# Kernel tuning notes

Hardware: AMD Instinct MI355X
Metric: run time of the kernel (lower is better)

Reference implementation:

```python
import jax, jax.numpy as jnp
import numpy as np

NUM_LAYERS = 4
EPS = 1e-8


def setup_inputs() -> dict:
    key = jax.random.key(0)
    ks = jax.random.split(key, 7)
    N, D, H = 8192, 1024, 4096
    return {
        "x": jax.random.normal(ks[0], (N, D), jnp.float32),
        "fc1_W": jax.random.normal(ks[1], (H, D), jnp.float32) * 0.02,
        "fc1_b": jax.random.normal(ks[2], (H,), jnp.float32) * 0.02,
        "fc2_W": jax.random.normal(ks[3], (D, H), jnp.float32) * 0.02,
        "fc2_b": jax.random.normal(ks[4], (D,), jnp.float32) * 0.02,
        "comp_W": jax.random.normal(ks[5], (NUM_LAYERS + 1, D, D), jnp.float32) * 0.03,
        "comp_b": jax.random.normal(ks[6], (NUM_LAYERS + 1, D), jnp.float32) * 0.03,
    }


def _block(x, fc1_W, fc1_b, fc2_W, fc2_b):
    # fc2(dropout(fc1(x))) in eval mode; relu is defined but never applied
    h = x @ fc1_W.T + fc1_b
    return h @ fc2_W.T + fc2_b


def _compute_loss(z, W, b):
    # out = Linear(z); per-row cosine_similarity(out_i.unsqueeze(1), out_i.unsqueeze(0))
    # reduces broadcast dim 1 -> vector c[j] = out[j]*sum(out) / max(|out[j]|*sqrt(y)*||out||, eps)
    # which torch broadcasts into constant rows of a [y,y] matrix; the
    # abs-diff accumulation over batch rows is then rank-1.
    out = z @ W.T + b                                # [N, y]
    y = out.shape[-1]
    S = out.sum(-1, keepdims=True)                   # [N, 1]
    n2 = jnp.sqrt((out * out).sum(-1, keepdims=True))  # [N, 1] row norms
    n1 = jnp.abs(out) * jnp.sqrt(jnp.asarray(y, out.dtype))  # [N, y]
    c = out * S / jnp.maximum(n1 * n2, EPS)          # [N, y]
    D = jnp.abs(c[1:] - c[:-1]).sum(0)               # [y]
    return jnp.broadcast_to(D, (y, y))               # [y, y]


def reference(x, fc1_W, fc1_b, fc2_W, fc2_b, comp_W, comp_b):
    inv = _block(x, fc1_W, fc1_b, fc2_W, fc2_b)
    loss = _compute_loss(inv, comp_W[0], comp_b[0])
    nxt = x - inv
    inv_total = inv
    for i in range(1, NUM_LAYERS + 1):
        inv_new = _block(nxt, fc1_W, fc1_b, fc2_W, fc2_b)
        inv_total = inv_total + inv_new
        loss = loss + _compute_loss(inv_new, comp_W[i], comp_b[i])
        nxt = nxt - inv_new
    return inv_total, nxt, loss
```

## Files before the change

kernel.cpp:

```cpp
#include <hip/hip_runtime.h>
#include <hip/hip_bf16.h>


#define NR 8192
#define DD 1024
#define HH 4096
#define NL 5
#define MSZ (DD * DD)

using bf16 = __hip_bfloat16;
typedef __attribute__((ext_vector_type(8))) short bf16x8;
typedef __attribute__((ext_vector_type(4))) float f32x4;


__device__ __forceinline__ void cvt4(const float* __restrict__ in, bf16* __restrict__ out, int i) {
  float4 v = ((const float4*)in)[i];
  union { bf16 b[4]; uint2 u; } u;
  u.b[0] = __float2bfloat16(v.x); u.b[1] = __float2bfloat16(v.y);
  u.b[2] = __float2bfloat16(v.z); u.b[3] = __float2bfloat16(v.w);
  ((uint2*)out)[i] = u.u;
}

#define NX4 (NR * DD / 4)
#define NF4 (DD * HH / 4)
#define NC4 (NL * MSZ / 4)
#define NS4 ((NL * DD + 2 * NL * NR) / 4)
#define NE4 (DD)

__global__ void prep_kernel(const float* __restrict__ x, const float* __restrict__ fc2_W,
                            const float* __restrict__ comp_W,
                            bf16* __restrict__ x_bf, bf16* __restrict__ fc2_bf,
                            bf16* __restrict__ compW_bf,
                            float* __restrict__ stats, float* __restrict__ ebuf) {
  int i = blockIdx.x * 256 + threadIdx.x;
  const int stride = gridDim.x * 256;
  const int total = NX4 + NF4 + NC4 + NS4 + NE4;
  const float4 z4 = {0.f, 0.f, 0.f, 0.f};
  for (; i < total; i += stride) {
    if (i < NX4) cvt4(x, x_bf, i);
    else if (i < NX4 + NF4) cvt4(fc2_W, fc2_bf, i - NX4);
    else if (i < NX4 + NF4 + NC4) cvt4(comp_W, compW_bf, i - NX4 - NF4);
    else if (i < NX4 + NF4 + NC4 + NS4) ((float4*)stats)[i - NX4 - NF4 - NC4] = z4;
    else ((float4*)ebuf)[i - NX4 - NF4 - NC4 - NS4] = z4;
  }
}

__global__ void transpose_cvt_kernel(const float* __restrict__ in, bf16* __restrict__ out) {
  __shared__ bf16 tile[64][74];
  int c0 = blockIdx.x * 64;
  int r0 = blockIdx.y * 64;
  int col = threadIdx.x & 63;
  int row4 = threadIdx.x >> 6;
  #pragma unroll
  for (int j = 0; j < 16; ++j) {
    int r = row4 * 16 + j;
    tile[r][col] = __float2bfloat16(in[(size_t)(r0 + r) * DD + c0 + col]);
  }
  __syncthreads();
  #pragma unroll
  for (int j = 0; j < 16; ++j) {
    int r = row4 * 16 + j;
    out[(size_t)(c0 + r) * HH + r0 + col] = tile[col][r];
  }
}

__global__ void cvec_kernel(const float* __restrict__ fc1_b, const float* __restrict__ fc2_W,
                            const float* __restrict__ fc2_b, float* __restrict__ c) {
  int j = blockIdx.x;
  float s = 0.f;
  for (int k = threadIdx.x; k < HH; k += 256) s += fc1_b[k] * fc2_W[(size_t)j * HH + k];
  for (int o = 32; o; o >>= 1) s += __shfl_down(s, o);
  __shared__ float red[4];
  if ((threadIdx.x & 63) == 0) red[threadIdx.x >> 6] = s;
  __syncthreads();
  if (threadIdx.x == 0) c[j] = red[0] + red[1] + red[2] + red[3] + fc2_b[j];
}

__global__ void mbuild_kernel(const float* __restrict__ Cp,
                              bf16* __restrict__ M, bf16* __restrict__ T, bf16* __restrict__ Tt) {
  __shared__ float tile[64][65];
  int n0 = blockIdx.x * 64, m0 = blockIdx.y * 64;
  int tn = threadIdx.x & 63, tm4 = threadIdx.x >> 6;
  #pragma unroll
  for (int j = 0; j < 16; ++j) {
    int m = tm4 * 16 + j;
    size_t idx = (size_t)(m0 + m) * DD + n0 + tn;
    float v = Cp[idx] + Cp[MSZ + idx] + Cp[2 * MSZ + idx] + Cp[3 * MSZ + idx];
    tile[m][tn] = v;
    float d = ((m0 + m) == (n0 + tn)) ? 1.f : 0.f;
    M[idx] = __float2bfloat16(v);
    T[idx] = __float2bfloat16(d - v);
  }
  __syncthreads();
  #pragma unroll
  for (int j = 0; j < 16; ++j) {
    int r = tm4 * 16 + j;
    float v = tile[tn][r];
    size_t idx = (size_t)(n0 + r) * DD + m0 + tn;
    float d = ((n0 + r) == (m0 + tn)) ? 1.f : 0.f;
    Tt[idx] = __float2bfloat16(d - v);
  }
}

__global__ void gemv4_kernel(const float* __restrict__ c, const bf16* __restrict__ Pw,
                             float* __restrict__ ebuf) {
  const int z = blockIdx.y;
  const int j = blockIdx.x * 256 + threadIdx.x;
  const bf16* P = Pw + (size_t)z * MSZ + j;
  const int k0 = blockIdx.z * 256;
  float s = 0.f;
  #pragma unroll 8
  for (int k = k0; k < k0 + 256; ++k) s += c[k] * __bfloat162float(P[(size_t)k * DD]);
  atomicAdd(&ebuf[z * DD + j], s);
}

__global__ void biasall_kernel(const float* __restrict__ cvec, const float* __restrict__ ebuf,
                               const float* __restrict__ comp_W, const float* __restrict__ comp_b,
                               float* __restrict__ biasall) {
  int z = blockIdx.y, j = blockIdx.x;
  if (z == 0) {
    if (threadIdx.x == 0)
      biasall[j] = cvec[j] + ebuf[j] + ebuf[DD + j] + ebuf[2 * DD + j] + ebuf[3 * DD + j];
    return;
  }
  int i = z - 1;
  const float* e = (i == 0) ? cvec : ebuf + (size_t)(i - 1) * DD;
  const float* wr = comp_W + (size_t)i * MSZ + (size_t)j * DD;
  float s = 0.f;
  for (int k = threadIdx.x; k < DD; k += 256) s += e[k] * wr[k];
  for (int o = 32; o; o >>= 1) s += __shfl_down(s, o);
  __shared__ float red[4];
  if ((threadIdx.x & 63) == 0) red[threadIdx.x >> 6] = s;
  __syncthreads();
  if (threadIdx.x == 0)
    biasall[(size_t)z * DD + j] = red[0] + red[1] + red[2] + red[3] + comp_b[(size_t)i * DD + j];
}


__device__ __forceinline__ void async16(const bf16* g, bf16* l) {
  __builtin_amdgcn_global_load_lds(
      (const __attribute__((address_space(1))) void*)g,
      (__attribute__((address_space(3))) void*)l, 16, 0, 0);
}

__device__ __forceinline__ void gemm_core_async(
    const bf16* __restrict__ A, const bf16* __restrict__ B,
    int kBeg, int kEnd, int lda, int ldb, int bm, int bn,
    bf16* As, bf16* Bs, f32x4 acc[4][4])
{
  const int tid  = threadIdx.x;
  const int lane = tid & 63;
  const int wave = tid >> 6;
  const int wm = (wave & 1) * 64;
  const int wn = (wave >> 1) * 64;
  const int lr = lane >> 3;
  const int lcol = ((lane & 7) ^ lr) * 8;
  const bf16* gA = A + (size_t)(bm + wave * 32 + lr) * lda + lcol;
  const bf16* gB = B + (size_t)(bn + wave * 32 + lr) * ldb + lcol;
  bf16* lA = As + wave * 32 * 64;
  bf16* lB = Bs + wave * 32 * 64;

  for (int k0 = kBeg; k0 < kEnd; k0 += 64) {
    #pragma unroll
    for (int it = 0; it < 4; ++it) {
      async16(gA + (size_t)(it * 8) * lda + k0, lA + it * 8 * 64);
      async16(gB + (size_t)(it * 8) * ldb + k0, lB + it * 8 * 64);
    }
    __syncthreads();
    #pragma unroll
    for (int ks = 0; ks < 2; ++ks) {
      bf16x8 av[4], bv[4];
      #pragma unroll
      for (int i = 0; i < 4; ++i) {
        const int rr = i * 16 + (lane & 15);
        const int cc = ((ks * 4 + (lane >> 4)) ^ (lane & 7)) * 8;
        av[i] = *(const bf16x8*)(As + (wm + rr) * 64 + cc);
        bv[i] = *(const bf16x8*)(Bs + (wn + rr) * 64 + cc);
      }
      #pragma unroll
      for (int i = 0; i < 4; ++i)
        #pragma unroll
        for (int j = 0; j < 4; ++j)
          acc[i][j] = __builtin_amdgcn_mfma_f32_16x16x32_bf16(av[i], bv[j], acc[i][j], 0, 0, 0);
    }
    __syncthreads();
  }
}

__device__ __forceinline__ void gemm_core64(
    const bf16* __restrict__ A, const bf16* __restrict__ B,
    int kBeg, int kEnd, int lda, int ldb, int bm, int bn,
    bf16* As, bf16* Bs, f32x4 acc[2][2])
{
  const int tid  = threadIdx.x;
  const int lane = tid & 63;
  const int wave = tid >> 6;
  const int wm = (wave & 1) * 32;
  const int wn = (wave >> 1) * 32;
  const int lr = lane >> 3;
  const int lcol = ((lane & 7) ^ lr) * 8;
  const bf16* gA = A + (size_t)(bm + wave * 16 + lr) * lda + lcol;
  const bf16* gB = B + (size_t)(bn + wave * 16 + lr) * ldb + lcol;
  bf16* lA = As + wave * 16 * 64;
  bf16* lB = Bs + wave * 16 * 64;

  for (int k0 = kBeg; k0 < kEnd; k0 += 64) {
    #pragma unroll
    for (int it = 0; it < 2; ++it) {
      async16(gA + (size_t)(it * 8) * lda + k0, lA + it * 8 * 64);
      async16(gB + (size_t)(it * 8) * ldb + k0, lB + it * 8 * 64);
    }
    __syncthreads();
    #pragma unroll
    for (int ks = 0; ks < 2; ++ks) {
      bf16x8 av[2], bv[2];
      #pragma unroll
      for (int i = 0; i < 2; ++i) {
        const int rr = i * 16 + (lane & 15);
        const int cc = ((ks * 4 + (lane >> 4)) ^ (lane & 7)) * 8;
        av[i] = *(const bf16x8*)(As + (wm + rr) * 64 + cc);
        bv[i] = *(const bf16x8*)(Bs + (wn + rr) * 64 + cc);
      }
      #pragma unroll
      for (int i = 0; i < 2; ++i)
        #pragma unroll
        for (int j = 0; j < 2; ++j)
          acc[i][j] = __builtin_amdgcn_mfma_f32_16x16x32_bf16(av[i], bv[j], acc[i][j], 0, 0, 0);
    }
    __syncthreads();
  }
}

#define GEMM_PROLOGUE \
  alignas(16) __shared__ bf16 As[128 * 64]; \
  alignas(16) __shared__ bf16 Bs[128 * 64]; \
  f32x4 acc[4][4] = {}; \
  const int lane = threadIdx.x & 63; \
  const int wm = ((threadIdx.x >> 6) & 1) * 64; \
  const int wn = ((threadIdx.x >> 6) >> 1) * 64;

#define GEMM_PROLOGUE64 \
  alignas(16) __shared__ bf16 As[64 * 64]; \
  alignas(16) __shared__ bf16 Bs[64 * 64]; \
  f32x4 acc[2][2] = {}; \
  const int lane = threadIdx.x & 63; \
  const int wm = ((threadIdx.x >> 6) & 1) * 32; \
  const int wn = ((threadIdx.x >> 6) >> 1) * 32;

__global__ __launch_bounds__(256, 4)
void gemm_splitk64(const bf16* __restrict__ A, const bf16* __restrict__ B, float* __restrict__ Cp) {
  GEMM_PROLOGUE64
  const int bm = blockIdx.y * 64, bn = blockIdx.x * 64;
  const int kb = blockIdx.z * (HH / 4);
  gemm_core64(A, B, kb, kb + HH / 4, HH, HH, bm, bn, As, Bs, acc);
  float* C = Cp + (size_t)blockIdx.z * MSZ;
  #pragma unroll
  for (int i = 0; i < 2; ++i)
    #pragma unroll
    for (int j = 0; j < 2; ++j) {
      const int col = bn + wn + j * 16 + (lane & 15);
      #pragma unroll
      for (int r = 0; r < 4; ++r) {
        const int row = bm + wm + i * 16 + (lane >> 4) * 4 + r;
        C[(size_t)row * DD + col] = acc[i][j][r];
      }
    }
}

__global__ __launch_bounds__(256, 4)
void gemm_dual64(const bf16* __restrict__ A, const bf16* __restrict__ B,
                 bf16* __restrict__ Ct, bf16* __restrict__ Cn) {
  GEMM_PROLOGUE64
  const int bm = blockIdx.y * 64, bn = blockIdx.x * 64;
  gemm_core64(A, B, 0, DD, DD, DD, bm, bn, As, Bs, acc);
  #pragma unroll
  for (int i = 0; i < 2; ++i)
    #pragma unroll
    for (int j = 0; j < 2; ++j) {
      const int col = bn + wn + j * 16 + (lane & 15);
      const int row0 = bm + wm + i * 16 + (lane >> 4) * 4;
      union { bf16 b[4]; uint2 u; } pk;
      #pragma unroll
      for (int r = 0; r < 4; ++r) {
        bf16 v = __float2bfloat16(acc[i][j][r]);
        pk.b[r] = v;
        Cn[(size_t)(row0 + r) * DD + col] = v;
      }
      *(uint2*)(&Ct[(size_t)col * DD + row0]) = pk.u;
    }
}

__global__ __launch_bounds__(256, 4)
void gemm_b64(const bf16* __restrict__ A0, long astr, const bf16* __restrict__ B0, long bstr,
              bf16* __restrict__ C0, long cstr) {
  GEMM_PROLOGUE64
  const int z = blockIdx.z;
  const bf16* A = A0 + (size_t)z * astr;
  const bf16* B = B0 + (size_t)z * bstr;
  bf16* C = C0 + (size_t)z * cstr;
  const int bm = blockIdx.y * 64, bn = blockIdx.x * 64;
  gemm_core64(A, B, 0, DD, DD, DD, bm, bn, As, Bs, acc);
  #pragma unroll
  for (int i = 0; i < 2; ++i)
    #pragma unroll
    for (int j = 0; j < 2; ++j) {
      const int col = bn + wn + j * 16 + (lane & 15);
      #pragma unroll
      for (int r = 0; r < 4; ++r) {
        const int row = bm + wm + i * 16 + (lane >> 4) * 4 + r;
        C[(size_t)row * DD + col] = __float2bfloat16(acc[i][j][r]);
      }
    }
}

__global__ __launch_bounds__(256, 4)
void gemm_t5_64(const bf16* __restrict__ A, const bf16* __restrict__ B,
                const bf16* __restrict__ Pw, bf16* __restrict__ Dl, bf16* __restrict__ Bbig0) {
  GEMM_PROLOGUE64
  const int bm = blockIdx.y * 64, bn = blockIdx.x * 64;
  gemm_core64(A, B, 0, DD, DD, DD, bm, bn, As, Bs, acc);
  #pragma unroll
  for (int i = 0; i < 2; ++i)
    #pragma unroll
    for (int j = 0; j < 2; ++j) {
      const int col = bn + wn + j * 16 + (lane & 15);
      const int row0 = bm + wm + i * 16 + (lane >> 4) * 4;
      union { bf16 b[4]; uint2 u; } pk;
      #pragma unroll
      for (int r = 0; r < 4; ++r) {
        const size_t idx = (size_t)(row0 + r) * DD + col;
        const float t1 = __bfloat162float(Pw[idx]);
        const float t2 = __bfloat162float(Pw[MSZ + idx]);
        const float t3 = __bfloat162float(Pw[2 * MSZ + idx]);
        const float t4 = __bfloat162float(Pw[3 * MSZ + idx]);
        const float t5 = acc[i][j][r];
        Dl[idx]           = __float2bfloat16(t1 - t2);
        Dl[MSZ + idx]     = __float2bfloat16(t2 - t3);
        Dl[2 * MSZ + idx] = __float2bfloat16(t3 - t4);
        Dl[3 * MSZ + idx] = __float2bfloat16(t4 - t5);
        pk.b[r] = __float2bfloat16((((row0 + r) == col) ? 1.f : 0.f) - t5);
      }
      *(uint2*)(&Bbig0[(size_t)col * DD + row0]) = pk.u;
    }
}

__global__ __launch_bounds__(256, 2)
void gemm_main(const bf16* __restrict__ A, const bf16* __restrict__ Bb,
               const float* __restrict__ biasall, const bf16* __restrict__ xb,
               float* __restrict__ invtot, float* __restrict__ nxtf,
               unsigned long long* __restrict__ sgn,
               float* __restrict__ Srow, float* __restrict__ Qrow) {
  GEMM_PROLOGUE
  const int bm = blockIdx.y * 128, bn = blockIdx.x * 128;
  gemm_core_async(A, Bb + (size_t)(bn >> 10) * MSZ, 0, DD, DD, DD, bm, bn & (DD - 1), As, Bs, acc);

  if (bn < DD) {
    #pragma unroll
    for (int i = 0; i < 4; ++i)
      #pragma unroll
      for (int j = 0; j < 4; ++j) {
        const int col = bn + wn + j * 16 + (lane & 15);
        const float bj = biasall[col];
        #pragma unroll
        for (int r = 0; r < 4; ++r) {
          const int row = bm + wm + i * 16 + (lane >> 4) * 4 + r;
          const float v = acc[i][j][r] + bj;
          const size_t idx = (size_t)row * DD + col;
          invtot[idx] = v;
          nxtf[idx] = __bfloat162float(xb[idx]) - v;
        }
      }
  } else {
    const int z = (bn >> 10) - 1;
    const int rb = bm >> 7;
    const int cb = (bn & (DD - 1)) >> 7;
    const int wave = threadIdx.x >> 6;
    unsigned long long keep = 0ULL;
    float sv[4][4] = {}, qv[4][4] = {};
    #pragma unroll
    for (int i = 0; i < 4; ++i)
      #pragma unroll
      for (int j = 0; j < 4; ++j) {
        const int colg = bn + wn + j * 16 + (lane & 15);
        const float bj = biasall[colg];
        #pragma unroll
        for (int r = 0; r < 4; ++r) {
          const float v = acc[i][j][r] + bj;
          const unsigned long long bal = __ballot(v < 0.f);
          if (lane == i * 16 + j * 4 + r) keep = bal;
          sv[i][r] += v;
          qv[i][r] += v * v;
        }
      }
    const size_t wbase = ((((size_t)z * 64 + rb) * 8 + cb) * 4 + wave) * 64;
    sgn[wbase + lane] = keep;
    #pragma unroll
    for (int i = 0; i < 4; ++i)
      #pragma unroll
      for (int r = 0; r < 4; ++r) {
        float s = sv[i][r], q = qv[i][r];
        #pragma unroll
        for (int off = 1; off < 16; off <<= 1) { s += __shfl_xor(s, off); q += __shfl_xor(q, off); }
        if ((lane & 15) == 0) {
          const int row = bm + wm + i * 16 + (lane >> 4) * 4 + r;
          atomicAdd(&Srow[(size_t)z * NR + row], s);
          atomicAdd(&Qrow[(size_t)z * NR + row], q);
        }
      }
  }
}


__global__ void losssign_kernel(const unsigned long long* __restrict__ sgn,
                                const float* __restrict__ Srow, const float* __restrict__ Qrow,
                                float* __restrict__ Dtot) {
  const int z = blockIdx.y;
  const int cg = blockIdx.x;
  const int n0 = blockIdx.z * 1024;
  __shared__ float rsh[1025];
  const float* S = Srow + (size_t)z * NR;
  const float* Q = Qrow + (size_t)z * NR;
  for (int t = threadIdx.x; t < 1025; t += 256) {
    int n = n0 + t; if (n > NR - 1) n = NR - 1;
    rsh[t] = S[n] * rsqrtf(Q[n]) * 0.03125f;
  }
  __syncthreads();
  const int c = threadIdx.x & 63;
  const int q = threadIdx.x >> 6;
  const int col = cg * 64 + c;
  const int cb = col >> 7;
  const int wsel = (col >> 6) & 1;
  const int jf = (col >> 4) & 3;
  const int c15 = col & 15;
  const size_t zbase = (size_t)z * 64 * 8 * 4 * 64;
  const int ns = n0 + q * 256;
  int ne = ns + 256; if (ne > NR - 1) ne = NR - 1;

  auto cval = [&](int n) -> float {
    const int rbk = n >> 7, nl = n & 127;
    const int wave = (nl >> 6) | (wsel << 1);
    const int i = (nl >> 4) & 3, rg = (nl >> 2) & 3, r = nl & 3;
    const size_t widx = zbase + ((((size_t)rbk * 8 + cb) * 4 + wave) * 64)
                      + i * 16 + jf * 4 + r;
    const unsigned long long wv = sgn[widx];
    const float rv = rsh[n - n0];
    return ((wv >> (rg * 16 + c15)) & 1ULL) ? -rv : rv;
  };

  float d = 0.f;
  float cprev = cval(ns);
  for (int n = ns + 1; n <= ne; ++n) {
    const float cn = cval(n);
    d += fabsf(cn - cprev);
    cprev = cn;
  }
  atomicAdd(&Dtot[z * DD + col], d);
}

__global__ void writeloss_kernel(const float* __restrict__ Dtot, float* __restrict__ out) {
  int idx = blockIdx.x * 256 + threadIdx.x;
  int j = idx & (DD - 1);
  out[idx] = Dtot[j] + Dtot[DD + j] + Dtot[2 * DD + j] + Dtot[3 * DD + j] + Dtot[4 * DD + j];
}


extern "C" void kernel_launch(void* const* d_in, const int* in_sizes, int n_in,
                              void* d_out, int out_size, void* d_ws, size_t ws_size,
                              hipStream_t stream) {
  const float* x      = (const float*)d_in[0];
  const float* fc1_W  = (const float*)d_in[1];
  const float* fc1_b  = (const float*)d_in[2];
  const float* fc2_W  = (const float*)d_in[3];
  const float* fc2_b  = (const float*)d_in[4];
  const float* comp_W = (const float*)d_in[5];
  const float* comp_b = (const float*)d_in[6];

  float* invtot  = (float*)d_out;
  float* nxtf    = invtot + (size_t)NR * DD;
  float* lossout = invtot + (size_t)2 * NR * DD;

  char* w = (char*)d_ws;
  auto alloc = [&](size_t bytes) { char* p = w; w += (bytes + 255) & ~(size_t)255; return p; };
  bf16* x_bf     = (bf16*)alloc((size_t)NR * DD * 2);
  bf16* fc1T_bf  = (bf16*)alloc((size_t)DD * HH * 2);
  bf16* fc2_bf   = (bf16*)alloc((size_t)DD * HH * 2);
  bf16* compW_bf = (bf16*)alloc((size_t)NL * MSZ * 2);
  bf16* Dbank    = (bf16*)alloc((size_t)5 * MSZ * 2);
  bf16* M_bf = Dbank;
  bf16* Dl   = Dbank + MSZ;
  bf16* Tt_buf   = (bf16*)alloc((size_t)2 * MSZ * 2);
  bf16* Pw       = (bf16*)alloc((size_t)4 * MSZ * 2);
  bf16* Bbig     = (bf16*)alloc((size_t)6 * MSZ * 2);
  unsigned long long* sgn = (unsigned long long*)alloc((size_t)NL * 64 * 8 * 4 * 64 * 8);
  float* Cp      = (float*)alloc((size_t)4 * MSZ * 4);
  float* cvec    = (float*)alloc(DD * 4);
  float* ebuf    = (float*)alloc((size_t)4 * DD * 4);
  float* biasall = (float*)alloc((size_t)6 * DD * 4);
  float* stats   = (float*)alloc((size_t)(NL * DD + 2 * NL * NR) * 4);
  float* Dtot = stats;
  float* Srow = stats + NL * DD;
  float* Qrow = Srow + (size_t)NL * NR;
  (void)ws_size; (void)in_sizes; (void)n_in; (void)out_size;

  prep_kernel<<<2048, 256, 0, stream>>>(x, fc2_W, comp_W, x_bf, fc2_bf, compW_bf, stats, ebuf);
  transpose_cvt_kernel<<<dim3(DD / 64, HH / 64), 256, 0, stream>>>(fc1_W, fc1T_bf);
  cvec_kernel<<<DD, 256, 0, stream>>>(fc1_b, fc2_W, fc2_b, cvec);

  gemm_splitk64<<<dim3(16, 16, 4), 256, 0, stream>>>(fc1T_bf, fc2_bf, Cp);
  mbuild_kernel<<<dim3(16, 16), 256, 0, stream>>>(Cp, M_bf, Pw, Tt_buf);
  gemm_dual64<<<dim3(16, 16), 256, 0, stream>>>(Pw, Tt_buf, Tt_buf + MSZ, Pw + MSZ);
  gemm_b64<<<dim3(16, 16, 2), 256, 0, stream>>>(Pw + MSZ, 0, Tt_buf, MSZ, Pw + 2 * MSZ, MSZ);
  gemm_t5_64<<<dim3(16, 16), 256, 0, stream>>>(Pw + 3 * MSZ, Tt_buf, Pw, Dl, Bbig);
  gemv4_kernel<<<dim3(4, 4, 4), 256, 0, stream>>>(cvec, Pw, ebuf);
  biasall_kernel<<<dim3(DD, 6), 256, 0, stream>>>(cvec, ebuf, comp_W, comp_b, biasall);
  gemm_b64<<<dim3(16, 16, NL), 256, 0, stream>>>(compW_bf, MSZ, Dbank, MSZ, Bbig + MSZ, MSZ);

  gemm_main<<<dim3(6 * DD / 128, NR / 128), 256, 0, stream>>>(
      x_bf, Bbig, biasall, x_bf, invtot, nxtf, sgn, Srow, Qrow);

  losssign_kernel<<<dim3(16, NL, 8), 256, 0, stream>>>(sgn, Srow, Qrow, Dtot);
  writeloss_kernel<<<MSZ / 256, 256, 0, stream>>>(Dtot, lossout);
}
```

Measured before the change: 483.1 us.

## Merge weight-precompute chain into one cooperative persistent kernel with grid syncs

Replaces the sequence of small weight-precompute kernels (split-K GEMM, M build, dual GEMM, batched GEMMs, t5 GEMM, gemv, bias) with a single cooperative kernel of 512 blocks separated by grid.sync, and merges the transpose and cvec kernels into one launch. The goal is to remove launch gaps and tail idle time between many short, under-occupied kernels and to overlap gemv/bias work with GEMM stages. Split-K for the first GEMM drops from 4 to 2 slices, which gives each block more serial work. The risk is that grid barriers and fixed per-block work assignment leave CUs idle where the separate launches could have packed more blocks.

```diff
diff --git a/kernel.cpp b/kernel.cpp
--- a/kernel.cpp
+++ b/kernel.cpp
@@ -1,5 +1,8 @@
 #include <hip/hip_runtime.h>
 #include <hip/hip_bf16.h>
+#include <hip/hip_cooperative_groups.h>
+
+namespace cg = cooperative_groups;
 
 
 #define NR 8192
@@ -45,95 +48,36 @@
   }
 }
 
-__global__ void transpose_cvt_kernel(const float* __restrict__ in, bf16* __restrict__ out) {
-  __shared__ bf16 tile[64][74];
-  int c0 = blockIdx.x * 64;
-  int r0 = blockIdx.y * 64;
-  int col = threadIdx.x & 63;
-  int row4 = threadIdx.x >> 6;
-  #pragma unroll
-  for (int j = 0; j < 16; ++j) {
-    int r = row4 * 16 + j;
-    tile[r][col] = __float2bfloat16(in[(size_t)(r0 + r) * DD + c0 + col]);
-  }
-  __syncthreads();
-  #pragma unroll
-  for (int j = 0; j < 16; ++j) {
-    int r = row4 * 16 + j;
-    out[(size_t)(c0 + r) * HH + r0 + col] = tile[col][r];
-  }
-}
-
-__global__ void cvec_kernel(const float* __restrict__ fc1_b, const float* __restrict__ fc2_W,
-                            const float* __restrict__ fc2_b, float* __restrict__ c) {
-  int j = blockIdx.x;
-  float s = 0.f;
-  for (int k = threadIdx.x; k < HH; k += 256) s += fc1_b[k] * fc2_W[(size_t)j * HH + k];
-  for (int o = 32; o; o >>= 1) s += __shfl_down(s, o);
-  __shared__ float red[4];
-  if ((threadIdx.x & 63) == 0) red[threadIdx.x >> 6] = s;
-  __syncthreads();
-  if (threadIdx.x == 0) c[j] = red[0] + red[1] + red[2] + red[3] + fc2_b[j];
-}
-
-__global__ void mbuild_kernel(const float* __restrict__ Cp,
-                              bf16* __restrict__ M, bf16* __restrict__ T, bf16* __restrict__ Tt) {
-  __shared__ float tile[64][65];
-  int n0 = blockIdx.x * 64, m0 = blockIdx.y * 64;
-  int tn = threadIdx.x & 63, tm4 = threadIdx.x >> 6;
-  #pragma unroll
-  for (int j = 0; j < 16; ++j) {
-    int m = tm4 * 16 + j;
-    size_t idx = (size_t)(m0 + m) * DD + n0 + tn;
-    float v = Cp[idx] + Cp[MSZ + idx] + Cp[2 * MSZ + idx] + Cp[3 * MSZ + idx];
-    tile[m][tn] = v;
-    float d = ((m0 + m) == (n0 + tn)) ? 1.f : 0.f;
-    M[idx] = __float2bfloat16(v);
-    T[idx] = __float2bfloat16(d - v);
-  }
-  __syncthreads();
-  #pragma unroll
-  for (int j = 0; j < 16; ++j) {
-    int r = tm4 * 16 + j;
-    float v = tile[tn][r];
-    size_t idx = (size_t)(n0 + r) * DD + m0 + tn;
-    float d = ((n0 + r) == (m0 + tn)) ? 1.f : 0.f;
-    Tt[idx] = __float2bfloat16(d - v);
-  }
-}
-
-__global__ void gemv4_kernel(const float* __restrict__ c, const bf16* __restrict__ Pw,
-                             float* __restrict__ ebuf) {
-  const int z = blockIdx.y;
-  const int j = blockIdx.x * 256 + threadIdx.x;
-  const bf16* P = Pw + (size_t)z * MSZ + j;
-  const int k0 = blockIdx.z * 256;
-  float s = 0.f;
-  #pragma unroll 8
-  for (int k = k0; k < k0 + 256; ++k) s += c[k] * __bfloat162float(P[(size_t)k * DD]);
-  atomicAdd(&ebuf[z * DD + j], s);
-}
-
-__global__ void biasall_kernel(const float* __restrict__ cvec, const float* __restrict__ ebuf,
-                               const float* __restrict__ comp_W, const float* __restrict__ comp_b,
-                               float* __restrict__ biasall) {
-  int z = blockIdx.y, j = blockIdx.x;
-  if (z == 0) {
-    if (threadIdx.x == 0)
-      biasall[j] = cvec[j] + ebuf[j] + ebuf[DD + j] + ebuf[2 * DD + j] + ebuf[3 * DD + j];
-    return;
-  }
-  int i = z - 1;
-  const float* e = (i == 0) ? cvec : ebuf + (size_t)(i - 1) * DD;
-  const float* wr = comp_W + (size_t)i * MSZ + (size_t)j * DD;
-  float s = 0.f;
-  for (int k = threadIdx.x; k < DD; k += 256) s += e[k] * wr[k];
-  for (int o = 32; o; o >>= 1) s += __shfl_down(s, o);
-  __shared__ float red[4];
-  if ((threadIdx.x & 63) == 0) red[threadIdx.x >> 6] = s;
-  __syncthreads();
-  if (threadIdx.x == 0)
-    biasall[(size_t)z * DD + j] = red[0] + red[1] + red[2] + red[3] + comp_b[(size_t)i * DD + j];
+__global__ void smallprep_kernel(const float* __restrict__ fc1_W, bf16* __restrict__ fc1T,
+                                 const float* __restrict__ fc1_b, const float* __restrict__ fc2_W,
+                                 const float* __restrict__ fc2_b, float* __restrict__ cvec) {
+  if (blockIdx.x < 1024) {
+    __shared__ bf16 tile[64][74];
+    const int c0 = (blockIdx.x & 15) * 64;
+    const int r0 = (blockIdx.x >> 4) * 64;
+    const int col = threadIdx.x & 63;
+    const int row4 = threadIdx.x >> 6;
+    #pragma unroll
+    for (int j = 0; j < 16; ++j) {
+      int r = row4 * 16 + j;
+      tile[r][col] = __float2bfloat16(fc1_W[(size_t)(r0 + r) * DD + c0 + col]);
+    }
+    __syncthreads();
+    #pragma unroll
+    for (int j = 0; j < 16; ++j) {
+      int r = row4 * 16 + j;
+      fc1T[(size_t)(c0 + r) * HH + r0 + col] = tile[col][r];
+    }
+  } else {
+    const int j = blockIdx.x - 1024;
+    float s = 0.f;
+    for (int k = threadIdx.x; k < HH; k += 256) s += fc1_b[k] * fc2_W[(size_t)j * HH + k];
+    for (int o = 32; o; o >>= 1) s += __shfl_down(s, o);
+    __shared__ float red[4];
+    if ((threadIdx.x & 63) == 0) red[threadIdx.x >> 6] = s;
+    __syncthreads();
+    if (threadIdx.x == 0) cvec[j] = red[0] + red[1] + red[2] + red[3] + fc2_b[j];
+  }
 }
 
 
@@ -142,6 +86,239 @@
       (const __attribute__((address_space(1))) void*)g,
       (__attribute__((address_space(3))) void*)l, 16, 0, 0);
 }
+
+__device__ __forceinline__ void gemm_core64(
+    const bf16* __restrict__ A, const bf16* __restrict__ B,
+    int kBeg, int kEnd, int lda, int ldb, int bm, int bn,
+    bf16* As, bf16* Bs, f32x4 acc[2][2])
+{
+  const int tid  = threadIdx.x;
+  const int lane = tid & 63;
+  const int wave = tid >> 6;
+  const int wm = (wave & 1) * 32;
+  const int wn = (wave >> 1) * 32;
+  const int lr = lane >> 3;
+  const int lcol = ((lane & 7) ^ lr) * 8;
+  const bf16* gA = A + (size_t)(bm + wave * 16 + lr) * lda + lcol;
+  const bf16* gB = B + (size_t)(bn + wave * 16 + lr) * ldb + lcol;
+  bf16* lA = As + wave * 16 * 64;
+  bf16* lB = Bs + wave * 16 * 64;
+
+  for (int k0 = kBeg; k0 < kEnd; k0 += 64) {
+    #pragma unroll
+    for (int it = 0; it < 2; ++it) {
+      async16(gA + (size_t)(it * 8) * lda + k0, lA + it * 8 * 64);
+      async16(gB + (size_t)(it * 8) * ldb + k0, lB + it * 8 * 64);
+    }
+    __syncthreads();
+    #pragma unroll
+    for (int ks = 0; ks < 2; ++ks) {
+      bf16x8 av[2], bv[2];
+      #pragma unroll
+      for (int i = 0; i < 2; ++i) {
+        const int rr = i * 16 + (lane & 15);
+        const int cc = ((ks * 4 + (lane >> 4)) ^ (lane & 7)) * 8;
+        av[i] = *(const bf16x8*)(As + (wm + rr) * 64 + cc);
+        bv[i] = *(const bf16x8*)(Bs + (wn + rr) * 64 + cc);
+      }
+      #pragma unroll
+      for (int i = 0; i < 2; ++i)
+        #pragma unroll
+        for (int j = 0; j < 2; ++j)
+          acc[i][j] = __builtin_amdgcn_mfma_f32_16x16x32_bf16(av[i], bv[j], acc[i][j], 0, 0, 0);
+    }
+    __syncthreads();
+  }
+}
+
+
+__global__ __launch_bounds__(256, 2)
+void mega_kernel(const bf16* __restrict__ fc1T, const bf16* __restrict__ fc2b,
+                 const float* __restrict__ cvec, const bf16* __restrict__ compWb,
+                 const float* __restrict__ comp_W, const float* __restrict__ comp_b,
+                 float* __restrict__ Cp, bf16* __restrict__ Dbank, bf16* __restrict__ Pw,
+                 bf16* __restrict__ Ttb, bf16* __restrict__ Bbig,
+                 float* __restrict__ ebuf, float* __restrict__ biasall) {
+  cg::grid_group grid = cg::this_grid();
+  __shared__ char smem[16640];
+  bf16* As = (bf16*)smem;
+  bf16* Bs = (bf16*)(smem + 8192);
+  const int b = blockIdx.x;
+  const int lane = threadIdx.x & 63;
+  const int wm = ((threadIdx.x >> 6) & 1) * 32;
+  const int wn = ((threadIdx.x >> 6) >> 1) * 32;
+
+  {
+    const int t = b >> 1, kh = b & 1;
+    const int m0 = (t >> 4) * 64, n0 = (t & 15) * 64;
+    f32x4 acc[2][2] = {};
+    gemm_core64(fc1T, fc2b, kh * (HH / 2), (kh + 1) * (HH / 2), HH, HH, m0, n0, As, Bs, acc);
+    float* C = Cp + (size_t)kh * MSZ;
+    #pragma unroll
+    for (int i = 0; i < 2; ++i)
+      #pragma unroll
+      for (int j = 0; j < 2; ++j) {
+        const int col = n0 + wn + j * 16 + (lane & 15);
+        #pragma unroll
+        for (int r = 0; r < 4; ++r) {
+          const int row = m0 + wm + i * 16 + (lane >> 4) * 4 + r;
+          C[(size_t)row * DD + col] = acc[i][j][r];
+        }
+      }
+  }
+  grid.sync();
+  if (b < 256) {
+    float (*tile)[65] = (float(*)[65])smem;
+    const int m0 = (b >> 4) * 64, n0 = (b & 15) * 64;
+    const int tn = threadIdx.x & 63, tm4 = threadIdx.x >> 6;
+    #pragma unroll
+    for (int j = 0; j < 16; ++j) {
+      const int m = tm4 * 16 + j;
+      const size_t idx = (size_t)(m0 + m) * DD + n0 + tn;
+      const float v = Cp[idx] + Cp[MSZ + idx];
+      tile[m][tn] = v;
+      const float d = ((m0 + m) == (n0 + tn)) ? 1.f : 0.f;
+      Dbank[idx] = __float2bfloat16(v);
+      Pw[idx]    = __float2bfloat16(d - v);
+    }
+    __syncthreads();
+    #pragma unroll
+    for (int j = 0; j < 16; ++j) {
+      const int r = tm4 * 16 + j;
+      const float v = tile[tn][r];
+      const size_t idx = (size_t)(n0 + r) * DD + m0 + tn;
+      const float d = ((n0 + r) == (m0 + tn)) ? 1.f : 0.f;
+      Ttb[idx] = __float2bfloat16(d - v);
+    }
+  }
+  grid.sync();
+  if (b < 256) {
+    const int m0 = (b >> 4) * 64, n0 = (b & 15) * 64;
+    f32x4 acc[2][2] = {};
+    gemm_core64(Pw, Ttb, 0, DD, DD, DD, m0, n0, As, Bs, acc);
+    #pragma unroll
+    for (int i = 0; i < 2; ++i)
+      #pragma unroll
+      for (int j = 0; j < 2; ++j) {
+        const int col = n0 + wn + j * 16 + (lane & 15);
+        const int row0 = m0 + wm + i * 16 + (lane >> 4) * 4;
+        union { bf16 h[4]; uint2 u; } pk;
+        #pragma unroll
+        for (int r = 0; r < 4; ++r) {
+          bf16 v = __float2bfloat16(acc[i][j][r]);
+          pk.h[r] = v;
+          Pw[MSZ + (size_t)(row0 + r) * DD + col] = v;
+        }
+        *(uint2*)(&Ttb[MSZ + (size_t)col * DD + row0]) = pk.u;
+      }
+  } else if (b < 272) {
+    const int idx = b - 256, jg = idx & 3, kg = idx >> 2;
+    const int j = jg * 256 + threadIdx.x, k0 = kg * 256;
+    float s = 0.f;
+    #pragma unroll 8
+    for (int k = k0; k < k0 + 256; ++k) s += cvec[k] * __bfloat162float(Pw[(size_t)k * DD + j]);
+    atomicAdd(&ebuf[j], s);
+  }
+  grid.sync();
+  {
+    const int z = b >> 8, t = b & 255;
+    const int m0 = (t >> 4) * 64, n0 = (t & 15) * 64;
+    f32x4 acc[2][2] = {};
+    gemm_core64(Pw + MSZ, Ttb + (size_t)z * MSZ, 0, DD, DD, DD, m0, n0, As, Bs, acc);
+    bf16* C = Pw + (size_t)(2 + z) * MSZ;
+    #pragma unroll
+    for (int i = 0; i < 2; ++i)
+      #pragma unroll
+      for (int j = 0; j < 2; ++j) {
+        const int col = n0 + wn + j * 16 + (lane & 15);
+        #pragma unroll
+        for (int r = 0; r < 4; ++r) {
+          const int row = m0 + wm + i * 16 + (lane >> 4) * 4 + r;
+          C[(size_t)row * DD + col] = __float2bfloat16(acc[i][j][r]);
+        }
+      }
+  }
+  grid.sync();
+  if (b < 256) {
+    const int m0 = (b >> 4) * 64, n0 = (b & 15) * 64;
+    f32x4 acc[2][2] = {};
+    gemm_core64(Pw + 3 * MSZ, Ttb, 0, DD, DD, DD, m0, n0, As, Bs, acc);
+    bf16* Dl = Dbank + MSZ;
+    #pragma unroll
+    for (int i = 0; i < 2; ++i)
+      #pragma unroll
+      for (int j = 0; j < 2; ++j) {
+        const int col = n0 + wn + j * 16 + (lane & 15);
+        const int row0 = m0 + wm + i * 16 + (lane >> 4) * 4;
+        union { bf16 h[4]; uint2 u; } pk;
+        #pragma unroll
+        for (int r = 0; r < 4; ++r) {
+          const size_t idx = (size_t)(row0 + r) * DD + col;
+          const float t1 = __bfloat162float(Pw[idx]);
+          const float t2 = __bfloat162float(Pw[MSZ + idx]);
+          const float t3 = __bfloat162float(Pw[2 * MSZ + idx]);
+          const float t4 = __bfloat162float(Pw[3 * MSZ + idx]);
+          const float t5 = acc[i][j][r];
+          Dl[idx]           = __float2bfloat16(t1 - t2);
+          Dl[MSZ + idx]     = __float2bfloat16(t2 - t3);
+          Dl[2 * MSZ + idx] = __float2bfloat16(t3 - t4);
+          Dl[3 * MSZ + idx] = __float2bfloat16(t4 - t5);
+          pk.h[r] = __float2bfloat16((((row0 + r) == col) ? 1.f : 0.f) - t5);
+        }
+        *(uint2*)(&Bbig[(size_t)col * DD + row0]) = pk.u;
+      }
+  } else if (b < 304) {
+    const int z = 1 + (b - 256) / 16, idx = (b - 256) % 16, jg = idx & 3, kg = idx >> 2;
+    const int j = jg * 256 + threadIdx.x, k0 = kg * 256;
+    const bf16* P = Pw + (size_t)z * MSZ;
+    float s = 0.f;
+    #pragma unroll 8
+    for (int k = k0; k < k0 + 256; ++k) s += cvec[k] * __bfloat162float(P[(size_t)k * DD + j]);
+    atomicAdd(&ebuf[(size_t)z * DD + j], s);
+  }
+  grid.sync();
+  for (int jb = b; jb < 1280; jb += 512) {
+    const int z = jb >> 8, t = jb & 255;
+    const int m0 = (t >> 4) * 64, n0 = (t & 15) * 64;
+    f32x4 acc[2][2] = {};
+    gemm_core64(compWb + (size_t)z * MSZ, Dbank + (size_t)z * MSZ, 0, DD, DD, DD,
+                m0, n0, As, Bs, acc);
+    bf16* C = Bbig + (size_t)(1 + z) * MSZ;
+    #pragma unroll
+    for (int i = 0; i < 2; ++i)
+      #pragma unroll
+      for (int j = 0; j < 2; ++j) {
+        const int col = n0 + wn + j * 16 + (lane & 15);
+        #pragma unroll
+        for (int r = 0; r < 4; ++r) {
+          const int row = m0 + wm + i * 16 + (lane >> 4) * 4 + r;
+          C[(size_t)row * DD + col] = __float2bfloat16(acc[i][j][r]);
+        }
+      }
+  }
+  float* red = (float*)smem;
+  for (int q = 0; q < 12; ++q) {
+    const int o = b * 12 + q;
+    const int z = o >> 10, j = o & 1023;
+    __syncthreads();
+    if (z == 0) {
+      if (threadIdx.x == 0)
+        biasall[j] = cvec[j] + ebuf[j] + ebuf[DD + j] + ebuf[2 * DD + j] + ebuf[3 * DD + j];
+    } else {
+      const int i = z - 1;
+      const float* e = (i == 0) ? cvec : ebuf + (size_t)(i - 1) * DD;
+      const float* wr2 = comp_W + (size_t)i * MSZ + (size_t)j * DD;
+      float s = 0.f;
+      for (int k = threadIdx.x; k < DD; k += 256) s += e[k] * wr2[k];
+      for (int o2 = 32; o2; o2 >>= 1) s += __shfl_down(s, o2);
+      if ((threadIdx.x & 63) == 0) red[threadIdx.x >> 6] = s;
+      __syncthreads();
+      if (threadIdx.x == 0)
+        biasall[(size_t)z * DD + j] = red[0] + red[1] + red[2] + red[3] + comp_b[(size_t)i * DD + j];
+    }
+  }
+}
+
 
 __device__ __forceinline__ void gemm_core_async(
     const bf16* __restrict__ A, const bf16* __restrict__ B,
@@ -187,50 +364,6 @@
   }
 }
 
-__device__ __forceinline__ void gemm_core64(
-    const bf16* __restrict__ A, const bf16* __restrict__ B,
-    int kBeg, int kEnd, int lda, int ldb, int bm, int bn,
-    bf16* As, bf16* Bs, f32x4 acc[2][2])
-{
-  const int tid  = threadIdx.x;
-  const int lane = tid & 63;
-  const int wave = tid >> 6;
-  const int wm = (wave & 1) * 32;
-  const int wn = (wave >> 1) * 32;
-  const int lr = lane >> 3;
-  const int lcol = ((lane & 7) ^ lr) * 8;
-  const bf16* gA = A + (size_t)(bm + wave * 16 + lr) * lda + lcol;
-  const bf16* gB = B + (size_t)(bn + wave * 16 + lr) * ldb + lcol;
-  bf16* lA = As + wave * 16 * 64;
-  bf16* lB = Bs + wave * 16 * 64;
-
-  for (int k0 = kBeg; k0 < kEnd; k0 += 64) {
-    #pragma unroll
-    for (int it = 0; it < 2; ++it) {
-      async16(gA + (size_t)(it * 8) * lda + k0, lA + it * 8 * 64);
-      async16(gB + (size_t)(it * 8) * ldb + k0, lB + it * 8 * 64);
-    }
-    __syncthreads();
-    #pragma unroll
-    for (int ks = 0; ks < 2; ++ks) {
-      bf16x8 av[2], bv[2];
-      #pragma unroll
-      for (int i = 0; i < 2; ++i) {
-        const int rr = i * 16 + (lane & 15);
-        const int cc = ((ks * 4 + (lane >> 4)) ^ (lane & 7)) * 8;
-        av[i] = *(const bf16x8*)(As + (wm + rr) * 64 + cc);
-        bv[i] = *(const bf16x8*)(Bs + (wn + rr) * 64 + cc);
-      }
-      #pragma unroll
-      for (int i = 0; i < 2; ++i)
-        #pragma unroll
-        for (int j = 0; j < 2; ++j)
-          acc[i][j] = __builtin_amdgcn_mfma_f32_16x16x32_bf16(av[i], bv[j], acc[i][j], 0, 0, 0);
-    }
-    __syncthreads();
-  }
-}
-
 #define GEMM_PROLOGUE \
   alignas(16) __shared__ bf16 As[128 * 64]; \
   alignas(16) __shared__ bf16 Bs[128 * 64]; \
@@ -238,111 +371,6 @@
   const int lane = threadIdx.x & 63; \
   const int wm = ((threadIdx.x >> 6) & 1) * 64; \
   const int wn = ((threadIdx.x >> 6) >> 1) * 64;
-
-#define GEMM_PROLOGUE64 \
-  alignas(16) __shared__ bf16 As[64 * 64]; \
-  alignas(16) __shared__ bf16 Bs[64 * 64]; \
-  f32x4 acc[2][2] = {}; \
-  const int lane = threadIdx.x & 63; \
-  const int wm = ((threadIdx.x >> 6) & 1) * 32; \
-  const int wn = ((threadIdx.x >> 6) >> 1) * 32;
-
-__global__ __launch_bounds__(256, 4)
-void gemm_splitk64(const bf16* __restrict__ A, const bf16* __restrict__ B, float* __restrict__ Cp) {
-  GEMM_PROLOGUE64
-  const int bm = blockIdx.y * 64, bn = blockIdx.x * 64;
-  const int kb = blockIdx.z * (HH / 4);
-  gemm_core64(A, B, kb, kb + HH / 4, HH, HH, bm, bn, As, Bs, acc);
-  float* C = Cp + (size_t)blockIdx.z * MSZ;
-  #pragma unroll
-  for (int i = 0; i < 2; ++i)
-    #pragma unroll
-    for (int j = 0; j < 2; ++j) {
-      const int col = bn + wn + j * 16 + (lane & 15);
-      #pragma unroll
-      for (int r = 0; r < 4; ++r) {
-        const int row = bm + wm + i * 16 + (lane >> 4) * 4 + r;
-        C[(size_t)row * DD + col] = acc[i][j][r];
-      }
-    }
-}
-
-__global__ __launch_bounds__(256, 4)
-void gemm_dual64(const bf16* __restrict__ A, const bf16* __restrict__ B,
-                 bf16* __restrict__ Ct, bf16* __restrict__ Cn) {
-  GEMM_PROLOGUE64
-  const int bm = blockIdx.y * 64, bn = blockIdx.x * 64;
-  gemm_core64(A, B, 0, DD, DD, DD, bm, bn, As, Bs, acc);
-  #pragma unroll
-  for (int i = 0; i < 2; ++i)
-    #pragma unroll
-    for (int j = 0; j < 2; ++j) {
-      const int col = bn + wn + j * 16 + (lane & 15);
-      const int row0 = bm + wm + i * 16 + (lane >> 4) * 4;
-      union { bf16 b[4]; uint2 u; } pk;
-      #pragma unroll
-      for (int r = 0; r < 4; ++r) {
-        bf16 v = __float2bfloat16(acc[i][j][r]);
-        pk.b[r] = v;
-        Cn[(size_t)(row0 + r) * DD + col] = v;
-      }
-      *(uint2*)(&Ct[(size_t)col * DD + row0]) = pk.u;
-    }
-}
-
-__global__ __launch_bounds__(256, 4)
-void gemm_b64(const bf16* __restrict__ A0, long astr, const bf16* __restrict__ B0, long bstr,
-              bf16* __restrict__ C0, long cstr) {
-  GEMM_PROLOGUE64
-  const int z = blockIdx.z;
-  const bf16* A = A0 + (size_t)z * astr;
-  const bf16* B = B0 + (size_t)z * bstr;
-  bf16* C = C0 + (size_t)z * cstr;
-  const int bm = blockIdx.y * 64, bn = blockIdx.x * 64;
-  gemm_core64(A, B, 0, DD, DD, DD, bm, bn, As, Bs, acc);
-  #pragma unroll
-  for (int i = 0; i < 2; ++i)
-    #pragma unroll
-    for (int j = 0; j < 2; ++j) {
-      const int col = bn + wn + j * 16 + (lane & 15);
-      #pragma unroll
-      for (int r = 0; r < 4; ++r) {
-        const int row = bm + wm + i * 16 + (lane >> 4) * 4 + r;
-        C[(size_t)row * DD + col] = __float2bfloat16(acc[i][j][r]);
-      }
-    }
-}
-
-__global__ __launch_bounds__(256, 4)
-void gemm_t5_64(const bf16* __restrict__ A, const bf16* __restrict__ B,
-                const bf16* __restrict__ Pw, bf16* __restrict__ Dl, bf16* __restrict__ Bbig0) {
-  GEMM_PROLOGUE64
-  const int bm = blockIdx.y * 64, bn = blockIdx.x * 64;
-  gemm_core64(A, B, 0, DD, DD, DD, bm, bn, As, Bs, acc);
-  #pragma unroll
-  for (int i = 0; i < 2; ++i)
-    #pragma unroll
-    for (int j = 0; j < 2; ++j) {
-      const int col = bn + wn + j * 16 + (lane & 15);
-      const int row0 = bm + wm + i * 16 + (lane >> 4) * 4;
-      union { bf16 b[4]; uint2 u; } pk;
-      #pragma unroll
-      for (int r = 0; r < 4; ++r) {
-        const size_t idx = (size_t)(row0 + r) * DD + col;
-        const float t1 = __bfloat162float(Pw[idx]);
-        const float t2 = __bfloat162float(Pw[MSZ + idx]);
-        const float t3 = __bfloat162float(Pw[2 * MSZ + idx]);
-        const float t4 = __bfloat162float(Pw[3 * MSZ + idx]);
-        const float t5 = acc[i][j][r];
-        Dl[idx]           = __float2bfloat16(t1 - t2);
-        Dl[MSZ + idx]     = __float2bfloat16(t2 - t3);
-        Dl[2 * MSZ + idx] = __float2bfloat16(t3 - t4);
-        Dl[3 * MSZ + idx] = __float2bfloat16(t4 - t5);
-        pk.b[r] = __float2bfloat16((((row0 + r) == col) ? 1.f : 0.f) - t5);
-      }
-      *(uint2*)(&Bbig0[(size_t)col * DD + row0]) = pk.u;
-    }
-}
 
 __global__ __launch_bounds__(256, 2)
 void gemm_main(const bf16* __restrict__ A, const bf16* __restrict__ Bb,
@@ -486,13 +514,11 @@
   bf16* fc2_bf   = (bf16*)alloc((size_t)DD * HH * 2);
   bf16* compW_bf = (bf16*)alloc((size_t)NL * MSZ * 2);
   bf16* Dbank    = (bf16*)alloc((size_t)5 * MSZ * 2);
-  bf16* M_bf = Dbank;
-  bf16* Dl   = Dbank + MSZ;
   bf16* Tt_buf   = (bf16*)alloc((size_t)2 * MSZ * 2);
   bf16* Pw       = (bf16*)alloc((size_t)4 * MSZ * 2);
   bf16* Bbig     = (bf16*)alloc((size_t)6 * MSZ * 2);
   unsigned long long* sgn = (unsigned long long*)alloc((size_t)NL * 64 * 8 * 4 * 64 * 8);
-  float* Cp      = (float*)alloc((size_t)4 * MSZ * 4);
+  float* Cp      = (float*)alloc((size_t)2 * MSZ * 4);
   float* cvec    = (float*)alloc(DD * 4);
   float* ebuf    = (float*)alloc((size_t)4 * DD * 4);
   float* biasall = (float*)alloc((size_t)6 * DD * 4);
@@ -503,21 +529,16 @@
   (void)ws_size; (void)in_sizes; (void)n_in; (void)out_size;
 
   prep_kernel<<<2048, 256, 0, stream>>>(x, fc2_W, comp_W, x_bf, fc2_bf, compW_bf, stats, ebuf);
-  transpose_cvt_kernel<<<dim3(DD / 64, HH / 64), 256, 0, stream>>>(fc1_W, fc1T_bf);
-  cvec_kernel<<<DD, 256, 0, stream>>>(fc1_b, fc2_W, fc2_b, cvec);
-
-  gemm_splitk64<<<dim3(16, 16, 4), 256, 0, stream>>>(fc1T_bf, fc2_bf, Cp);
-  mbuild_kernel<<<dim3(16, 16), 256, 0, stream>>>(Cp, M_bf, Pw, Tt_buf);
-  gemm_dual64<<<dim3(16, 16), 256, 0, stream>>>(Pw, Tt_buf, Tt_buf + MSZ, Pw + MSZ);
-  gemm_b64<<<dim3(16, 16, 2), 256, 0, stream>>>(Pw + MSZ, 0, Tt_buf, MSZ, Pw + 2 * MSZ, MSZ);
-  gemm_t5_64<<<dim3(16, 16), 256, 0, stream>>>(Pw + 3 * MSZ, Tt_buf, Pw, Dl, Bbig);
-  gemv4_kernel<<<dim3(4, 4, 4), 256, 0, stream>>>(cvec, Pw, ebuf);
-  biasall_kernel<<<dim3(DD, 6), 256, 0, stream>>>(cvec, ebuf, comp_W, comp_b, biasall);
-  gemm_b64<<<dim3(16, 16, NL), 256, 0, stream>>>(compW_bf, MSZ, Dbank, MSZ, Bbig + MSZ, MSZ);
-
+  smallprep_kernel<<<2048, 256, 0, stream>>>(fc1_W, fc1T_bf, fc1_b, fc2_W, fc2_b, cvec);
+  {
+    void* args[] = {
+      (void*)&fc1T_bf, (void*)&fc2_bf, (void*)&cvec, (void*)&compW_bf,
+      (void*)&comp_W, (void*)&comp_b, (void*)&Cp, (void*)&Dbank, (void*)&Pw,
+      (void*)&Tt_buf, (void*)&Bbig, (void*)&ebuf, (void*)&biasall };
+    hipLaunchCooperativeKernel((void*)mega_kernel, dim3(512), dim3(256), args, 0, stream);
+  }
   gemm_main<<<dim3(6 * DD / 128, NR / 128), 256, 0, stream>>>(
       x_bf, Bbig, biasall, x_bf, invtot, nxtf, sgn, Srow, Qrow);
-
   losssign_kernel<<<dim3(16, NL, 8), 256, 0, stream>>>(sgn, Srow, Qrow, Dtot);
   writeloss_kernel<<<MSZ / 256, 256, 0, stream>>>(Dtot, lossout);
 }
```

Result: slower. 810.8 us (+67.8%).
